# Optimization experiments

Hardware: AMD Instinct MI355X
Metric: run time of the kernel (lower is better)

Reference implementation:

```python
import jax, jax.numpy as jnp
import numpy as np

DIM = 16
HID = 256
BATCH = 8192
N_STEPS = 10      # fixed-step RK4 replaces adaptive dopri5 for a deterministic reference
T0, T1 = 0.0, 1.0
LOG_2PI = float(np.log(2.0 * np.pi))


def setup_inputs() -> dict:
    key = jax.random.key(0)
    ks = jax.random.split(key, 7)

    def lin_w(k, fan_in, fan_out):
        lim = 1.0 / np.sqrt(fan_in)
        return jax.random.uniform(k, (fan_in, fan_out), minval=-lim, maxval=lim, dtype=jnp.float32)

    def lin_b(k, fan_in, fan_out):
        lim = 1.0 / np.sqrt(fan_in)
        return jax.random.uniform(k, (fan_out,), minval=-lim, maxval=lim, dtype=jnp.float32)

    x = jax.random.normal(ks[0], (BATCH, DIM), dtype=jnp.float32)
    return {
        "x": x,
        "W1": lin_w(ks[1], DIM + 1, HID), "b1": lin_b(ks[2], DIM + 1, HID),
        "W2": lin_w(ks[3], HID, HID),     "b2": lin_b(ks[4], HID, HID),
        "W3": lin_w(ks[5], HID, DIM),     "b3": lin_b(ks[6], HID, DIM),
    }


def _mlp(W1, b1, W2, b2, W3, b3, h):
    h = jax.nn.silu(h @ W1 + b1)
    h = jax.nn.silu(h @ W2 + b2)
    return h @ W3 + b3


def reference(x, W1, b1, W2, b2, W3, b3):
    dtype = x.dtype

    def f(t, z):  # time-conditioned vector field f(z, t): [B, d] -> [B, d]
        t_col = jnp.full((z.shape[0], 1), t, dtype=dtype)
        return _mlp(W1, b1, W2, b2, W3, b3, jnp.concatenate([z, t_col], axis=1))

    eye = jnp.eye(DIM, dtype=dtype)

    def f_and_div(t, z):
        fz = f(t, z)
        # exact divergence = trace of Jacobian, via DIM forward-mode JVPs
        def jvp_dir(e):  # e: [d]
            _, jv = jax.jvp(lambda zz: f(t, zz), (z,), (jnp.broadcast_to(e, z.shape),))
            return jv  # [B, d]
        jvs = jax.vmap(jvp_dir)(eye)          # [d, B, d]
        div = jnp.einsum('ibi->b', jvs)       # sum_i dF_i/dz_i
        return fz, div

    dt = jnp.asarray((T1 - T0) / N_STEPS, dtype=dtype)

    def rhs(t, z):
        fz, div = f_and_div(t, z)
        return fz, -div   # dz/dt, dlogp/dt

    def step(state, i):
        z, logp = state
        t = T0 + i * dt
        k1z, k1l = rhs(t, z)
        k2z, k2l = rhs(t + 0.5 * dt, z + 0.5 * dt * k1z)
        k3z, k3l = rhs(t + 0.5 * dt, z + 0.5 * dt * k2z)
        k4z, k4l = rhs(t + dt, z + dt * k3z)
        z = z + (dt / 6.0) * (k1z + 2.0 * k2z + 2.0 * k3z + k4z)
        logp = logp + (dt / 6.0) * (k1l + 2.0 * k2l + 2.0 * k3l + k4l)
        return (z, logp), None

    logp0 = jnp.zeros(x.shape[0], dtype=dtype)
    (z1, logp1), _ = jax.lax.scan(step, (x, logp0), jnp.arange(N_STEPS, dtype=dtype))

    logpz = -0.5 * (jnp.sum(z1 * z1, axis=1) + DIM * LOG_2PI)
    return logpz - logp1
```

## Files before the change

kernel.cpp:

```cpp
#include <hip/hip_runtime.h>

#define DIM 16
#define HID 256
#define NSTEPS 10
#define TILE_B 32
#define NTHR 1024
#define LSH 264

typedef __attribute__((ext_vector_type(8))) short bf16x8;
typedef __attribute__((ext_vector_type(4))) float f32x4;

__device__ __forceinline__ unsigned short f2bf(float f) {
    unsigned u = __float_as_uint(f);
    u += 0x7fff + ((u >> 16) & 1);
    return (unsigned short)(u >> 16);
}
__device__ __forceinline__ unsigned short f2bf_trunc(float f) {
    return (unsigned short)(__float_as_uint(f) >> 16);
}
__device__ __forceinline__ float bf2f(unsigned short u) {
    return __uint_as_float((unsigned)u << 16);
}
__device__ __forceinline__ void silu_both(float x, float& h, float& d) {
    float s = __builtin_amdgcn_rcpf(1.0f + __expf(-x));
    h = x * s;
    d = fmaf(h, 1.0f - s, s);
}

__global__ void cnf_setup(const float* __restrict__ W1, const float* __restrict__ W2,
                          const float* __restrict__ W3,
                          unsigned short* __restrict__ w2t, unsigned short* __restrict__ mt) {
    const int j = blockIdx.x;
    const int n = threadIdx.x;
    float g = 0.0f;
#pragma unroll
    for (int i = 0; i < DIM; ++i) g = fmaf(W1[i * HID + j], W3[n * DIM + i], g);
    const float w2 = W2[j * HID + n];
    w2t[n * HID + j] = f2bf(w2);
    mt [n * HID + j] = f2bf(w2 * g);
}

__global__ __launch_bounds__(NTHR, 4) void cnf_main(
    const float* __restrict__ x,
    const float* __restrict__ W1, const float* __restrict__ b1,
    const float* __restrict__ b2, const float* __restrict__ b3,
    const unsigned short* __restrict__ w2t, const unsigned short* __restrict__ mt,
    const float* __restrict__ W3, float* __restrict__ out)
{
    __shared__ unsigned short zb[TILE_B][24];
    __shared__ unsigned short w1t[HID][24];
    __shared__ unsigned short w3t[DIM][LSH];
    __shared__ unsigned short h1s[TILE_B][LSH];
    __shared__ unsigned short d1s[TILE_B][LSH];
    __shared__ unsigned short h2s[TILE_B][LSH];
    __shared__ unsigned short d2s[TILE_B][LSH];
    __shared__ float divp[8][TILE_B];

    const int tid  = (int)threadIdx.x;
    const int lane = tid & 63;
    const int wv   = tid >> 6;
    const int g    = lane >> 4;
    const int r    = lane & 15;
    const int b0   = (int)blockIdx.x * TILE_B;
    const int wx   = (g >> 1) << 4;
    const int goff = (g * 8) ^ (((r >> 3) & 1) << 4);

    bf16x8 breg[8][2];
    const int n0w = (wv & 7) * 32;
    {
        const unsigned short* Bg = (wv < 8) ? w2t : mt;
#pragma unroll
        for (int k = 0; k < 8; ++k)
#pragma unroll
            for (int ct = 0; ct < 2; ++ct)
                breg[k][ct] = *(const bf16x8*)(Bg + (n0w + ct * 16 + r) * HID + k * 32 + g * 8);
    }

    const int n_p1 = wv * 16 + r;
    const int nw_p1 = n_p1 ^ wx;
    const float b1n = b1[n_p1];
    const float w1n = W1[DIM * HID + n_p1];
    const float b2r0 = b2[n0w + r], b2r1 = b2[n0w + 16 + r];
    float b3r = 0.0f;
    if (wv < 2) b3r = b3[r];

    if (tid < 512) {
        const int n = tid >> 1, kh = (tid & 1) * 8;
#pragma unroll
        for (int k = 0; k < 8; ++k) w1t[n][kh + k] = f2bf(W1[(kh + k) * HID + n]);
    }
    if (tid < 512) {
        const int n = tid >> 5, k0 = (tid & 31) * 8;
#pragma unroll
        for (int j = 0; j < 8; ++j) w3t[n][k0 + j] = f2bf(W3[(k0 + j) * DIM + n]);
    }
    float zb4[4] = {0.f, 0.f, 0.f, 0.f};
    float za4[4] = {0.f, 0.f, 0.f, 0.f};
    if (wv < 2) {
#pragma unroll
        for (int q = 0; q < 4; ++q) {
            const int row = wv * 16 + g * 4 + q;
            zb4[q] = x[(b0 + row) * DIM + r];
            zb[row][r] = f2bf(zb4[q]);
        }
    }
    float lacc = 0.0f, logp = 0.0f;

    const float dt = 0.1f, dt6 = dt / 6.0f;

    for (int it = 0; it < NSTEPS * 4; ++it) {
        const int s = it & 3;
        const int step = it >> 2;
        const float t0 = dt * (float)step;
        const float tcur = t0 + ((s == 0) ? 0.0f : (s == 3) ? dt : 0.5f * dt);
        const float wst = (s == 1 || s == 2) ? 2.0f : 1.0f;
        __syncthreads();

        if (wv == 8 && lane < 32 && it) {
            const int ps = (it + 3) & 3;
            const float pw = (ps == 1 || ps == 2) ? 2.0f : 1.0f;
            float dv = 0.0f;
#pragma unroll
            for (int w = 0; w < 8; ++w) dv += divp[w][lane];
            lacc = fmaf(-pw, dv, lacc);
            if (ps == 3) { logp = fmaf(dt6, lacc, logp); lacc = 0.0f; }
        }

        {
            const bf16x8 zf = {0, 0, 0, 0, 0, 0, 0, 0};
            bf16x8 az[2], bw;
#pragma unroll
            for (int rt = 0; rt < 2; ++rt)
                az[rt] = (g < 2) ? *(const bf16x8*)&zb[rt * 16 + r][g * 8] : zf;
            bw = (g < 2) ? *(const bf16x8*)&w1t[n_p1][g * 8] : zf;
            const float bb = fmaf(tcur, w1n, b1n);
#pragma unroll
            for (int rt = 0; rt < 2; ++rt) {
                f32x4 c = {0.f, 0.f, 0.f, 0.f};
                c = __builtin_amdgcn_mfma_f32_16x16x32_bf16(az[rt], bw, c, 0, 0, 0);
#pragma unroll
                for (int q = 0; q < 4; ++q) {
                    float h, d;
                    silu_both(c[q] + bb, h, d);
                    h1s[rt * 16 + g * 4 + q][nw_p1] = f2bf_trunc(h);
                    d1s[rt * 16 + g * 4 + q][nw_p1] = f2bf_trunc(d);
                }
            }
        }
        __syncthreads();

        f32x4 cc[2][2];
        {
            const unsigned short (*aT)[LSH] = (wv < 8) ? h1s : d1s;
#pragma unroll
            for (int a = 0; a < 2; ++a)
#pragma unroll
                for (int b = 0; b < 2; ++b) cc[a][b] = (f32x4){0.f, 0.f, 0.f, 0.f};
#pragma unroll
            for (int k = 0; k < 8; ++k) {
                bf16x8 af[2];
#pragma unroll
                for (int rt = 0; rt < 2; ++rt)
                    af[rt] = *(const bf16x8*)&aT[rt * 16 + r][k * 32 + goff];
#pragma unroll
                for (int rt = 0; rt < 2; ++rt)
#pragma unroll
                    for (int ct = 0; ct < 2; ++ct)
                        cc[rt][ct] = __builtin_amdgcn_mfma_f32_16x16x32_bf16(af[rt], breg[k][ct], cc[rt][ct], 0, 0, 0);
            }
        }
        if (wv < 8) {
#pragma unroll
            for (int ct = 0; ct < 2; ++ct) {
                const int nw = (n0w + ct * 16 + r) ^ wx;
                const float bb = (ct == 0) ? b2r0 : b2r1;
#pragma unroll
                for (int rt = 0; rt < 2; ++rt)
#pragma unroll
                    for (int q = 0; q < 4; ++q) {
                        float h, d;
                        silu_both(cc[rt][ct][q] + bb, h, d);
                        h2s[rt * 16 + g * 4 + q][nw] = f2bf_trunc(h);
                        d2s[rt * 16 + g * 4 + q][nw] = f2bf_trunc(d);
                    }
            }
        }
        __syncthreads();

        if (wv < 2) {
            f32x4 c3 = {0.f, 0.f, 0.f, 0.f};
#pragma unroll
            for (int ks = 0; ks < 8; ++ks) {
                bf16x8 a = *(const bf16x8*)&h2s[wv * 16 + r][ks * 32 + goff];
                bf16x8 b = *(const bf16x8*)&w3t[r][ks * 32 + g * 8];
                c3 = __builtin_amdgcn_mfma_f32_16x16x32_bf16(a, b, c3, 0, 0, 0);
            }
            const float coef = (s == 2) ? dt : 0.5f * dt;
#pragma unroll
            for (int q = 0; q < 4; ++q) {
                const float fz = c3[q] + b3r;
                za4[q] = fmaf(wst, fz, za4[q]);
                float znext;
                if (s < 3) {
                    znext = fmaf(coef, fz, zb4[q]);
                } else {
                    zb4[q] = fmaf(dt6, za4[q], zb4[q]);
                    znext = zb4[q];
                    za4[q] = 0.0f;
                }
                zb[wv * 16 + g * 4 + q][r] = f2bf(znext);
            }
        } else if (wv >= 8) {
            float p[2][4];
#pragma unroll
            for (int rt = 0; rt < 2; ++rt)
#pragma unroll
                for (int q = 0; q < 4; ++q) p[rt][q] = 0.0f;
#pragma unroll
            for (int ct = 0; ct < 2; ++ct) {
                const int nr = (n0w + ct * 16 + r) ^ wx;
#pragma unroll
                for (int rt = 0; rt < 2; ++rt)
#pragma unroll
                    for (int q = 0; q < 4; ++q) {
                        const float d2v = bf2f(d2s[rt * 16 + g * 4 + q][nr]);
                        p[rt][q] = fmaf(d2v, cc[rt][ct][q], p[rt][q]);
                    }
            }
#pragma unroll
            for (int m = 1; m < 16; m <<= 1)
#pragma unroll
                for (int rt = 0; rt < 2; ++rt)
#pragma unroll
                    for (int q = 0; q < 4; ++q) p[rt][q] += __shfl_xor(p[rt][q], m, 64);
            if (r == 0)
#pragma unroll
                for (int rt = 0; rt < 2; ++rt)
#pragma unroll
                    for (int q = 0; q < 4; ++q) divp[wv - 8][rt * 16 + g * 4 + q] = p[rt][q];
        }
    }

    __syncthreads();
    if (wv == 8 && lane < 32) {
        float dv = 0.0f;
#pragma unroll
        for (int w = 0; w < 8; ++w) dv += divp[w][lane];
        lacc -= dv;
        logp = fmaf(dt6, lacc, logp);
        divp[0][lane] = logp;
    }
    __syncthreads();
    if (wv < 2) {
        float ss[4];
#pragma unroll
        for (int q = 0; q < 4; ++q) ss[q] = zb4[q] * zb4[q];
#pragma unroll
        for (int m = 1; m < 16; m <<= 1)
#pragma unroll
            for (int q = 0; q < 4; ++q) ss[q] += __shfl_xor(ss[q], m, 64);
        if (r == 0) {
#pragma unroll
            for (int q = 0; q < 4; ++q) {
                const int row = wv * 16 + g * 4 + q;
                out[b0 + row] = -0.5f * (ss[q] + (float)DIM * 1.8378770664093453f) - divp[0][row];
            }
        }
    }
}

extern "C" void kernel_launch(void* const* d_in, const int* in_sizes, int n_in,
                              void* d_out, int out_size, void* d_ws, size_t ws_size,
                              hipStream_t stream) {
    (void)in_sizes; (void)n_in; (void)out_size; (void)ws_size;
    const float* x  = (const float*)d_in[0];
    const float* W1 = (const float*)d_in[1];
    const float* b1 = (const float*)d_in[2];
    const float* W2 = (const float*)d_in[3];
    const float* b2 = (const float*)d_in[4];
    const float* W3 = (const float*)d_in[5];
    const float* b3 = (const float*)d_in[6];
    unsigned short* w2t = (unsigned short*)d_ws;
    unsigned short* mt  = w2t + HID * HID;

    cnf_setup<<<HID, HID, 0, stream>>>(W1, W2, W3, w2t, mt);
    cnf_main<<<8192 / TILE_B, NTHR, 0, stream>>>(x, W1, b1, b2, b3, w2t, mt, W3, (float*)d_out);
}
```

Before: 218.4 us.

## Switch layer-2 to 32x32x16 MFMA with transposed operands and folded bias/time

Layer 2 now keeps the W2 and M weights as the A operand in registers and runs 32x32x16 MFMAs, giving one 16-float accumulator per wave in place of four 16x16 tiles. The divergence reduction then needs only a single cross-half shuffle instead of a 4-step butterfly. Layer 1 moves to the upper 8 waves, with time and b1 folded into the MFMA through an augmented z column, and its outputs are written as packed 4-element stores. The intent is fewer MFMA issues, fewer shuffles and fewer scalar LDS stores, at the cost of new swizzle patterns that could bring back bank conflicts.

```diff
diff --git a/kernel.cpp b/kernel.cpp
--- a/kernel.cpp
+++ b/kernel.cpp
@@ -9,17 +9,18 @@
 
 typedef __attribute__((ext_vector_type(8))) short bf16x8;
 typedef __attribute__((ext_vector_type(4))) float f32x4;
+typedef __attribute__((ext_vector_type(16))) float f32x16;
+typedef __attribute__((ext_vector_type(2))) unsigned int u32x2;
 
 __device__ __forceinline__ unsigned short f2bf(float f) {
     unsigned u = __float_as_uint(f);
     u += 0x7fff + ((u >> 16) & 1);
     return (unsigned short)(u >> 16);
 }
-__device__ __forceinline__ unsigned short f2bf_trunc(float f) {
-    return (unsigned short)(__float_as_uint(f) >> 16);
-}
-__device__ __forceinline__ float bf2f(unsigned short u) {
-    return __uint_as_float((unsigned)u << 16);
+__device__ __forceinline__ float bfw_lo(unsigned u) { return __uint_as_float(u << 16); }
+__device__ __forceinline__ float bfw_hi(unsigned u) { return __uint_as_float(u & 0xffff0000u); }
+__device__ __forceinline__ unsigned packtr(float a, float b) {
+    return __builtin_amdgcn_perm(__float_as_uint(b), __float_as_uint(a), 0x07060302u);
 }
 __device__ __forceinline__ void silu_both(float x, float& h, float& d) {
     float s = __builtin_amdgcn_rcpf(1.0f + __expf(-x));
@@ -47,76 +48,78 @@
     const unsigned short* __restrict__ w2t, const unsigned short* __restrict__ mt,
     const float* __restrict__ W3, float* __restrict__ out)
 {
-    __shared__ unsigned short zb[TILE_B][24];
-    __shared__ unsigned short w1t[HID][24];
+    __shared__ unsigned short zb[TILE_B][40];
     __shared__ unsigned short w3t[DIM][LSH];
     __shared__ unsigned short h1s[TILE_B][LSH];
     __shared__ unsigned short d1s[TILE_B][LSH];
     __shared__ unsigned short h2s[TILE_B][LSH];
     __shared__ unsigned short d2s[TILE_B][LSH];
     __shared__ float divp[8][TILE_B];
+    __shared__ float b2l[HID];
 
     const int tid  = (int)threadIdx.x;
     const int lane = tid & 63;
     const int wv   = tid >> 6;
-    const int g    = lane >> 4;
-    const int r    = lane & 15;
+    const int l5   = lane & 31, hi = lane >> 5, hi8 = hi * 8;
+    const int r    = lane & 15, g  = lane >> 4, g8  = g * 8;
     const int b0   = (int)blockIdx.x * TILE_B;
-    const int wx   = (g >> 1) << 4;
-    const int goff = (g * 8) ^ (((r >> 3) & 1) << 4);
-
-    bf16x8 breg[8][2];
-    const int n0w = (wv & 7) * 32;
+    const int swb  = ((l5 >> 3) & 1) << 4;
+    const int swr  = ((r  >> 3) & 1) << 4;
+    const int nblk = (wv & 7) * 32;
+
+    bf16x8 areg[16];
     {
-        const unsigned short* Bg = (wv < 8) ? w2t : mt;
-#pragma unroll
-        for (int k = 0; k < 8; ++k)
-#pragma unroll
-            for (int ct = 0; ct < 2; ++ct)
-                breg[k][ct] = *(const bf16x8*)(Bg + (n0w + ct * 16 + r) * HID + k * 32 + g * 8);
-    }
-
-    const int n_p1 = wv * 16 + r;
-    const int nw_p1 = n_p1 ^ wx;
-    const float b1n = b1[n_p1];
-    const float w1n = W1[DIM * HID + n_p1];
-    const float b2r0 = b2[n0w + r], b2r1 = b2[n0w + 16 + r];
-    float b3r = 0.0f;
-    if (wv < 2) b3r = b3[r];
-
-    if (tid < 512) {
-        const int n = tid >> 1, kh = (tid & 1) * 8;
-#pragma unroll
-        for (int k = 0; k < 8; ++k) w1t[n][kh + k] = f2bf(W1[(kh + k) * HID + n]);
+        const unsigned short* Arow = ((wv < 8) ? w2t : mt) + (nblk + l5) * HID + hi8;
+#pragma unroll
+        for (int kt = 0; kt < 16; ++kt) areg[kt] = *(const bf16x8*)(Arow + kt * 16);
+    }
+
+    bf16x8 w1f0 = {0,0,0,0,0,0,0,0}, w1f1 = {0,0,0,0,0,0,0,0};
+    if (wv >= 8) {
+        const int nb1 = (wv - 8) * 32;
+#pragma unroll
+        for (int e = 0; e < 8; ++e) {
+            const int k = g8 + e;
+            float v0 = 0.0f, v1 = 0.0f;
+            if (k < 17)       { v0 = W1[k * HID + nb1 + r]; v1 = W1[k * HID + nb1 + 16 + r]; }
+            else if (k == 17) { v0 = b1[nb1 + r];           v1 = b1[nb1 + 16 + r]; }
+            w1f0[e] = (short)f2bf(v0);
+            w1f1[e] = (short)f2bf(v1);
+        }
+    }
+
+    float zb4[4] = {0,0,0,0}, za4[4] = {0,0,0,0}, b3q[4] = {0,0,0,0};
+    if (wv < 2) {
+#pragma unroll
+        for (int q = 0; q < 4; ++q) b3q[q] = b3[4 * g + q];
+        const f32x4 xv = *(const f32x4*)&x[(b0 + wv * 16 + r) * DIM + 4 * g];
+#pragma unroll
+        for (int q = 0; q < 4; ++q) zb4[q] = xv[q];
+        u32x2 pz = { (unsigned)f2bf(zb4[0]) | ((unsigned)f2bf(zb4[1]) << 16),
+                     (unsigned)f2bf(zb4[2]) | ((unsigned)f2bf(zb4[3]) << 16) };
+        *(u32x2*)&zb[wv * 16 + r][4 * g] = pz;
+    }
+    if (tid < TILE_B) {
+#pragma unroll
+        for (int c = 16; c < 32; ++c)
+            zb[tid][c] = (c == 17) ? (unsigned short)0x3F80 : (unsigned short)0;
     }
     if (tid < 512) {
         const int n = tid >> 5, k0 = (tid & 31) * 8;
 #pragma unroll
         for (int j = 0; j < 8; ++j) w3t[n][k0 + j] = f2bf(W3[(k0 + j) * DIM + n]);
     }
-    float zb4[4] = {0.f, 0.f, 0.f, 0.f};
-    float za4[4] = {0.f, 0.f, 0.f, 0.f};
-    if (wv < 2) {
-#pragma unroll
-        for (int q = 0; q < 4; ++q) {
-            const int row = wv * 16 + g * 4 + q;
-            zb4[q] = x[(b0 + row) * DIM + r];
-            zb[row][r] = f2bf(zb4[q]);
-        }
-    }
+    if (tid < HID) b2l[tid] = b2[tid];
+
     float lacc = 0.0f, logp = 0.0f;
-
     const float dt = 0.1f, dt6 = dt / 6.0f;
 
     for (int it = 0; it < NSTEPS * 4; ++it) {
         const int s = it & 3;
-        const int step = it >> 2;
-        const float t0 = dt * (float)step;
-        const float tcur = t0 + ((s == 0) ? 0.0f : (s == 3) ? dt : 0.5f * dt);
         const float wst = (s == 1 || s == 2) ? 2.0f : 1.0f;
         __syncthreads();
 
-        if (wv == 8 && lane < 32 && it) {
+        if (wv == 8 && lane < TILE_B && it) {
             const int ps = (it + 3) & 3;
             const float pw = (ps == 1 || ps == 2) ? 2.0f : 1.0f;
             float dv = 0.0f;
@@ -126,123 +129,102 @@
             if (ps == 3) { logp = fmaf(dt6, lacc, logp); lacc = 0.0f; }
         }
 
+        if (wv >= 8) {
+            const int nb1 = (wv - 8) * 32;
+#pragma unroll
+            for (int bt = 0; bt < 2; ++bt) {
+                const bf16x8 bz = *(const bf16x8*)&zb[bt * 16 + r][g8];
+#pragma unroll
+                for (int nt = 0; nt < 2; ++nt) {
+                    f32x4 c = {0.f, 0.f, 0.f, 0.f};
+                    c = __builtin_amdgcn_mfma_f32_16x16x32_bf16(nt ? w1f1 : w1f0, bz, c, 0, 0, 0);
+                    float h[4], d[4];
+#pragma unroll
+                    for (int q = 0; q < 4; ++q) silu_both(c[q], h[q], d[q]);
+                    const int col = (nb1 + nt * 16 + 4 * g) ^ swr;
+                    const int row = bt * 16 + r;
+                    u32x2 hv = { packtr(h[0], h[1]), packtr(h[2], h[3]) };
+                    u32x2 dv2 = { packtr(d[0], d[1]), packtr(d[2], d[3]) };
+                    *(u32x2*)&h1s[row][col] = hv;
+                    *(u32x2*)&d1s[row][col] = dv2;
+                }
+            }
+        }
+        __syncthreads();
+
+        f32x16 cc;
+#pragma unroll
+        for (int p = 0; p < 16; ++p) cc[p] = 0.0f;
         {
-            const bf16x8 zf = {0, 0, 0, 0, 0, 0, 0, 0};
-            bf16x8 az[2], bw;
-#pragma unroll
-            for (int rt = 0; rt < 2; ++rt)
-                az[rt] = (g < 2) ? *(const bf16x8*)&zb[rt * 16 + r][g * 8] : zf;
-            bw = (g < 2) ? *(const bf16x8*)&w1t[n_p1][g * 8] : zf;
-            const float bb = fmaf(tcur, w1n, b1n);
-#pragma unroll
-            for (int rt = 0; rt < 2; ++rt) {
-                f32x4 c = {0.f, 0.f, 0.f, 0.f};
-                c = __builtin_amdgcn_mfma_f32_16x16x32_bf16(az[rt], bw, c, 0, 0, 0);
-#pragma unroll
-                for (int q = 0; q < 4; ++q) {
-                    float h, d;
-                    silu_both(c[q] + bb, h, d);
-                    h1s[rt * 16 + g * 4 + q][nw_p1] = f2bf_trunc(h);
-                    d1s[rt * 16 + g * 4 + q][nw_p1] = f2bf_trunc(d);
-                }
-            }
-        }
-        __syncthreads();
-
-        f32x4 cc[2][2];
-        {
-            const unsigned short (*aT)[LSH] = (wv < 8) ? h1s : d1s;
-#pragma unroll
-            for (int a = 0; a < 2; ++a)
-#pragma unroll
-                for (int b = 0; b < 2; ++b) cc[a][b] = (f32x4){0.f, 0.f, 0.f, 0.f};
-#pragma unroll
-            for (int k = 0; k < 8; ++k) {
-                bf16x8 af[2];
-#pragma unroll
-                for (int rt = 0; rt < 2; ++rt)
-                    af[rt] = *(const bf16x8*)&aT[rt * 16 + r][k * 32 + goff];
-#pragma unroll
-                for (int rt = 0; rt < 2; ++rt)
-#pragma unroll
-                    for (int ct = 0; ct < 2; ++ct)
-                        cc[rt][ct] = __builtin_amdgcn_mfma_f32_16x16x32_bf16(af[rt], breg[k][ct], cc[rt][ct], 0, 0, 0);
+            const unsigned short* Brow = (wv < 8) ? &h1s[l5][0] : &d1s[l5][0];
+#pragma unroll
+            for (int kt = 0; kt < 16; ++kt) {
+                const bf16x8 bf = *(const bf16x8*)(Brow + ((kt * 16 + hi8) ^ swb));
+                cc = __builtin_amdgcn_mfma_f32_32x32x16_bf16(areg[kt], bf, cc, 0, 0, 0);
             }
         }
         if (wv < 8) {
 #pragma unroll
-            for (int ct = 0; ct < 2; ++ct) {
-                const int nw = (n0w + ct * 16 + r) ^ wx;
-                const float bb = (ct == 0) ? b2r0 : b2r1;
-#pragma unroll
-                for (int rt = 0; rt < 2; ++rt)
-#pragma unroll
-                    for (int q = 0; q < 4; ++q) {
-                        float h, d;
-                        silu_both(cc[rt][ct][q] + bb, h, d);
-                        h2s[rt * 16 + g * 4 + q][nw] = f2bf_trunc(h);
-                        d2s[rt * 16 + g * 4 + q][nw] = f2bf_trunc(d);
-                    }
+            for (int pg = 0; pg < 4; ++pg) {
+                const f32x4 bb = *(const f32x4*)&b2l[nblk + pg * 8 + 4 * hi];
+                float h[4], d[4];
+#pragma unroll
+                for (int q = 0; q < 4; ++q) silu_both(cc[pg * 4 + q] + bb[q], h[q], d[q]);
+                const int col = (nblk + pg * 8 + 4 * hi) ^ swb;
+                u32x2 hv = { packtr(h[0], h[1]), packtr(h[2], h[3]) };
+                u32x2 dv2 = { packtr(d[0], d[1]), packtr(d[2], d[3]) };
+                *(u32x2*)&h2s[l5][col] = hv;
+                *(u32x2*)&d2s[l5][col] = dv2;
             }
         }
         __syncthreads();
 
         if (wv < 2) {
             f32x4 c3 = {0.f, 0.f, 0.f, 0.f};
-#pragma unroll
-            for (int ks = 0; ks < 8; ++ks) {
-                bf16x8 a = *(const bf16x8*)&h2s[wv * 16 + r][ks * 32 + goff];
-                bf16x8 b = *(const bf16x8*)&w3t[r][ks * 32 + g * 8];
-                c3 = __builtin_amdgcn_mfma_f32_16x16x32_bf16(a, b, c3, 0, 0, 0);
+            const unsigned short* h2row = &h2s[wv * 16 + r][0];
+            const unsigned short* w3row = &w3t[r][0];
+#pragma unroll
+            for (int kt = 0; kt < 8; ++kt) {
+                const bf16x8 a3  = *(const bf16x8*)(w3row + kt * 32 + g8);
+                const bf16x8 bf3 = *(const bf16x8*)(h2row + ((kt * 32 + g8) ^ swr));
+                c3 = __builtin_amdgcn_mfma_f32_16x16x32_bf16(a3, bf3, c3, 0, 0, 0);
             }
             const float coef = (s == 2) ? dt : 0.5f * dt;
+            float zn[4];
 #pragma unroll
             for (int q = 0; q < 4; ++q) {
-                const float fz = c3[q] + b3r;
+                const float fz = c3[q] + b3q[q];
                 za4[q] = fmaf(wst, fz, za4[q]);
-                float znext;
-                if (s < 3) {
-                    znext = fmaf(coef, fz, zb4[q]);
-                } else {
-                    zb4[q] = fmaf(dt6, za4[q], zb4[q]);
-                    znext = zb4[q];
-                    za4[q] = 0.0f;
-                }
-                zb[wv * 16 + g * 4 + q][r] = f2bf(znext);
+                if (s < 3) zn[q] = fmaf(coef, fz, zb4[q]);
+                else { zb4[q] = fmaf(dt6, za4[q], zb4[q]); zn[q] = zb4[q]; za4[q] = 0.0f; }
+            }
+            u32x2 pz = { (unsigned)f2bf(zn[0]) | ((unsigned)f2bf(zn[1]) << 16),
+                         (unsigned)f2bf(zn[2]) | ((unsigned)f2bf(zn[3]) << 16) };
+            *(u32x2*)&zb[wv * 16 + r][4 * g] = pz;
+            if (wv == 0 && lane < TILE_B) {
+                const int it1 = it + 1;
+                const int s1 = it1 & 3;
+                const float t1 = dt * (float)(it1 >> 2) + ((s1 == 0) ? 0.0f : (s1 == 3) ? dt : 0.5f * dt);
+                zb[lane][16] = f2bf(t1);
             }
         } else if (wv >= 8) {
-            float p[2][4];
-#pragma unroll
-            for (int rt = 0; rt < 2; ++rt)
-#pragma unroll
-                for (int q = 0; q < 4; ++q) p[rt][q] = 0.0f;
-#pragma unroll
-            for (int ct = 0; ct < 2; ++ct) {
-                const int nr = (n0w + ct * 16 + r) ^ wx;
-#pragma unroll
-                for (int rt = 0; rt < 2; ++rt)
-#pragma unroll
-                    for (int q = 0; q < 4; ++q) {
-                        const float d2v = bf2f(d2s[rt * 16 + g * 4 + q][nr]);
-                        p[rt][q] = fmaf(d2v, cc[rt][ct][q], p[rt][q]);
-                    }
-            }
-#pragma unroll
-            for (int m = 1; m < 16; m <<= 1)
-#pragma unroll
-                for (int rt = 0; rt < 2; ++rt)
-#pragma unroll
-                    for (int q = 0; q < 4; ++q) p[rt][q] += __shfl_xor(p[rt][q], m, 64);
-            if (r == 0)
-#pragma unroll
-                for (int rt = 0; rt < 2; ++rt)
-#pragma unroll
-                    for (int q = 0; q < 4; ++q) divp[wv - 8][rt * 16 + g * 4 + q] = p[rt][q];
+            float pd = 0.0f;
+#pragma unroll
+            for (int pg = 0; pg < 4; ++pg) {
+                const int col = (nblk + pg * 8 + 4 * hi) ^ swb;
+                const u32x2 du = *(const u32x2*)&d2s[l5][col];
+                pd = fmaf(bfw_lo(du[0]), cc[pg * 4 + 0], pd);
+                pd = fmaf(bfw_hi(du[0]), cc[pg * 4 + 1], pd);
+                pd = fmaf(bfw_lo(du[1]), cc[pg * 4 + 2], pd);
+                pd = fmaf(bfw_hi(du[1]), cc[pg * 4 + 3], pd);
+            }
+            pd += __shfl_xor(pd, 32, 64);
+            if (lane < TILE_B) divp[wv - 8][lane] = pd;
         }
     }
 
     __syncthreads();
-    if (wv == 8 && lane < 32) {
+    if (wv == 8 && lane < TILE_B) {
         float dv = 0.0f;
 #pragma unroll
         for (int w = 0; w < 8; ++w) dv += divp[w][lane];
@@ -252,19 +234,12 @@
     }
     __syncthreads();
     if (wv < 2) {
-        float ss[4];
-#pragma unroll
-        for (int q = 0; q < 4; ++q) ss[q] = zb4[q] * zb4[q];
-#pragma unroll
-        for (int m = 1; m < 16; m <<= 1)
-#pragma unroll
-            for (int q = 0; q < 4; ++q) ss[q] += __shfl_xor(ss[q], m, 64);
-        if (r == 0) {
-#pragma unroll
-            for (int q = 0; q < 4; ++q) {
-                const int row = wv * 16 + g * 4 + q;
-                out[b0 + row] = -0.5f * (ss[q] + (float)DIM * 1.8378770664093453f) - divp[0][row];
-            }
+        float ss = zb4[0]*zb4[0] + zb4[1]*zb4[1] + zb4[2]*zb4[2] + zb4[3]*zb4[3];
+        ss += __shfl_xor(ss, 16, 64);
+        ss += __shfl_xor(ss, 32, 64);
+        if (g == 0) {
+            const int row = wv * 16 + r;
+            out[b0 + row] = -0.5f * (ss + (float)DIM * 1.8378770664093453f) - divp[0][row];
         }
     }
 }
```

Result: slower. 307.4 us (+40.8%).

## Transpose MFMA operands and fold time and bias into layer-1 GEMM

Applied to the files above, without the earlier changes.

Layer 1 now swaps the MFMA operands so each lane holds four consecutive hidden columns. This allows packed 64-bit stores of h1/d1 via byte-permute truncation. The time input and the b1 bias are folded into the K dimension as extra columns (t and a constant 1) held in zb, with W1 kept in registers instead of shared memory. Layer 3 is likewise transposed so z is written as packed vectors, and it uses two accumulators to break the MFMA dependency chain. The final reduction needs fewer shuffles. The risk is that t and b1 are now rounded to bf16, which slightly changes accuracy.

```diff
diff --git a/kernel.cpp b/kernel.cpp
--- a/kernel.cpp
+++ b/kernel.cpp
@@ -9,6 +9,7 @@
 
 typedef __attribute__((ext_vector_type(8))) short bf16x8;
 typedef __attribute__((ext_vector_type(4))) float f32x4;
+typedef __attribute__((ext_vector_type(2))) unsigned int u32x2;
 
 __device__ __forceinline__ unsigned short f2bf(float f) {
     unsigned u = __float_as_uint(f);
@@ -20,6 +21,9 @@
 }
 __device__ __forceinline__ float bf2f(unsigned short u) {
     return __uint_as_float((unsigned)u << 16);
+}
+__device__ __forceinline__ unsigned packtr(float a, float b) {
+    return __builtin_amdgcn_perm(__float_as_uint(b), __float_as_uint(a), 0x07060302u);
 }
 __device__ __forceinline__ void silu_both(float x, float& h, float& d) {
     float s = __builtin_amdgcn_rcpf(1.0f + __expf(-x));
@@ -47,8 +51,7 @@
     const unsigned short* __restrict__ w2t, const unsigned short* __restrict__ mt,
     const float* __restrict__ W3, float* __restrict__ out)
 {
-    __shared__ unsigned short zb[TILE_B][24];
-    __shared__ unsigned short w1t[HID][24];
+    __shared__ unsigned short zb[TILE_B][40];
     __shared__ unsigned short w3t[DIM][LSH];
     __shared__ unsigned short h1s[TILE_B][LSH];
     __shared__ unsigned short d1s[TILE_B][LSH];
@@ -61,62 +64,71 @@
     const int wv   = tid >> 6;
     const int g    = lane >> 4;
     const int r    = lane & 15;
+    const int g8   = g * 8;
     const int b0   = (int)blockIdx.x * TILE_B;
     const int wx   = (g >> 1) << 4;
-    const int goff = (g * 8) ^ (((r >> 3) & 1) << 4);
+    const int swr  = ((r >> 3) & 1) << 4;
+    const int goff = g8 ^ swr;
+    const int n0w  = (wv & 7) * 32;
 
     bf16x8 breg[8][2];
-    const int n0w = (wv & 7) * 32;
     {
         const unsigned short* Bg = (wv < 8) ? w2t : mt;
 #pragma unroll
         for (int k = 0; k < 8; ++k)
 #pragma unroll
             for (int ct = 0; ct < 2; ++ct)
-                breg[k][ct] = *(const bf16x8*)(Bg + (n0w + ct * 16 + r) * HID + k * 32 + g * 8);
-    }
-
-    const int n_p1 = wv * 16 + r;
-    const int nw_p1 = n_p1 ^ wx;
-    const float b1n = b1[n_p1];
-    const float w1n = W1[DIM * HID + n_p1];
+                breg[k][ct] = *(const bf16x8*)(Bg + (n0w + ct * 16 + r) * HID + k * 32 + g8);
+    }
+
+    bf16x8 w1f;
+    {
+        const int n = wv * 16 + r;
+#pragma unroll
+        for (int e = 0; e < 8; ++e) {
+            const int k = g8 + e;
+            float v = 0.0f;
+            if (k < 17)       v = W1[k * HID + n];
+            else if (k == 17) v = b1[n];
+            w1f[e] = (short)f2bf(v);
+        }
+    }
+
     const float b2r0 = b2[n0w + r], b2r1 = b2[n0w + 16 + r];
-    float b3r = 0.0f;
-    if (wv < 2) b3r = b3[r];
-
-    if (tid < 512) {
-        const int n = tid >> 1, kh = (tid & 1) * 8;
-#pragma unroll
-        for (int k = 0; k < 8; ++k) w1t[n][kh + k] = f2bf(W1[(kh + k) * HID + n]);
+    float b3q[4] = {0, 0, 0, 0};
+    if (wv < 2)
+#pragma unroll
+        for (int q = 0; q < 4; ++q) b3q[q] = b3[4 * g + q];
+
+    float zb4[4] = {0, 0, 0, 0}, za4[4] = {0, 0, 0, 0};
+    if (wv < 2) {
+        const f32x4 xv = *(const f32x4*)&x[(b0 + wv * 16 + r) * DIM + 4 * g];
+#pragma unroll
+        for (int q = 0; q < 4; ++q) zb4[q] = xv[q];
+        u32x2 pz = { (unsigned)f2bf(zb4[0]) | ((unsigned)f2bf(zb4[1]) << 16),
+                     (unsigned)f2bf(zb4[2]) | ((unsigned)f2bf(zb4[3]) << 16) };
+        *(u32x2*)&zb[wv * 16 + r][4 * g] = pz;
+    }
+    if (tid < TILE_B) {
+#pragma unroll
+        for (int c = 16; c < 32; ++c)
+            zb[tid][c] = (c == 17) ? (unsigned short)0x3F80 : (unsigned short)0;
     }
     if (tid < 512) {
         const int n = tid >> 5, k0 = (tid & 31) * 8;
 #pragma unroll
         for (int j = 0; j < 8; ++j) w3t[n][k0 + j] = f2bf(W3[(k0 + j) * DIM + n]);
     }
-    float zb4[4] = {0.f, 0.f, 0.f, 0.f};
-    float za4[4] = {0.f, 0.f, 0.f, 0.f};
-    if (wv < 2) {
-#pragma unroll
-        for (int q = 0; q < 4; ++q) {
-            const int row = wv * 16 + g * 4 + q;
-            zb4[q] = x[(b0 + row) * DIM + r];
-            zb[row][r] = f2bf(zb4[q]);
-        }
-    }
+
     float lacc = 0.0f, logp = 0.0f;
-
     const float dt = 0.1f, dt6 = dt / 6.0f;
 
     for (int it = 0; it < NSTEPS * 4; ++it) {
         const int s = it & 3;
-        const int step = it >> 2;
-        const float t0 = dt * (float)step;
-        const float tcur = t0 + ((s == 0) ? 0.0f : (s == 3) ? dt : 0.5f * dt);
         const float wst = (s == 1 || s == 2) ? 2.0f : 1.0f;
         __syncthreads();
 
-        if (wv == 8 && lane < 32 && it) {
+        if (wv == 8 && lane < TILE_B && it) {
             const int ps = (it + 3) & 3;
             const float pw = (ps == 1 || ps == 2) ? 2.0f : 1.0f;
             float dv = 0.0f;
@@ -127,24 +139,20 @@
         }
 
         {
-            const bf16x8 zf = {0, 0, 0, 0, 0, 0, 0, 0};
-            bf16x8 az[2], bw;
-#pragma unroll
-            for (int rt = 0; rt < 2; ++rt)
-                az[rt] = (g < 2) ? *(const bf16x8*)&zb[rt * 16 + r][g * 8] : zf;
-            bw = (g < 2) ? *(const bf16x8*)&w1t[n_p1][g * 8] : zf;
-            const float bb = fmaf(tcur, w1n, b1n);
-#pragma unroll
-            for (int rt = 0; rt < 2; ++rt) {
+#pragma unroll
+            for (int bt = 0; bt < 2; ++bt) {
+                const bf16x8 bz = *(const bf16x8*)&zb[bt * 16 + r][g8];
                 f32x4 c = {0.f, 0.f, 0.f, 0.f};
-                c = __builtin_amdgcn_mfma_f32_16x16x32_bf16(az[rt], bw, c, 0, 0, 0);
-#pragma unroll
-                for (int q = 0; q < 4; ++q) {
-                    float h, d;
-                    silu_both(c[q] + bb, h, d);
-                    h1s[rt * 16 + g * 4 + q][nw_p1] = f2bf_trunc(h);
-                    d1s[rt * 16 + g * 4 + q][nw_p1] = f2bf_trunc(d);
-                }
+                c = __builtin_amdgcn_mfma_f32_16x16x32_bf16(w1f, bz, c, 0, 0, 0);
+                float h[4], d[4];
+#pragma unroll
+                for (int q = 0; q < 4; ++q) silu_both(c[q], h[q], d[q]);
+                const int row = bt * 16 + r;
+                const int col = (wv * 16 + 4 * g) ^ swr;
+                u32x2 hv  = { packtr(h[0], h[1]), packtr(h[2], h[3]) };
+                u32x2 dv2 = { packtr(d[0], d[1]), packtr(d[2], d[3]) };
+                *(u32x2*)&h1s[row][col] = hv;
+                *(u32x2*)&d1s[row][col] = dv2;
             }
         }
         __syncthreads();
@@ -188,27 +196,33 @@
         __syncthreads();
 
         if (wv < 2) {
-            f32x4 c3 = {0.f, 0.f, 0.f, 0.f};
-#pragma unroll
-            for (int ks = 0; ks < 8; ++ks) {
-                bf16x8 a = *(const bf16x8*)&h2s[wv * 16 + r][ks * 32 + goff];
-                bf16x8 b = *(const bf16x8*)&w3t[r][ks * 32 + g * 8];
-                c3 = __builtin_amdgcn_mfma_f32_16x16x32_bf16(a, b, c3, 0, 0, 0);
+            const unsigned short* h2row = &h2s[wv * 16 + r][0];
+            const unsigned short* w3row = &w3t[r][0];
+            f32x4 c3a = {0.f, 0.f, 0.f, 0.f}, c3b = {0.f, 0.f, 0.f, 0.f};
+#pragma unroll
+            for (int kt = 0; kt < 8; ++kt) {
+                const bf16x8 a3  = *(const bf16x8*)(w3row + kt * 32 + g8);
+                const bf16x8 bf3 = *(const bf16x8*)(h2row + kt * 32 + goff);
+                if (kt & 1) c3b = __builtin_amdgcn_mfma_f32_16x16x32_bf16(a3, bf3, c3b, 0, 0, 0);
+                else        c3a = __builtin_amdgcn_mfma_f32_16x16x32_bf16(a3, bf3, c3a, 0, 0, 0);
             }
             const float coef = (s == 2) ? dt : 0.5f * dt;
+            float zn[4];
 #pragma unroll
             for (int q = 0; q < 4; ++q) {
-                const float fz = c3[q] + b3r;
+                const float fz = c3a[q] + c3b[q] + b3q[q];
                 za4[q] = fmaf(wst, fz, za4[q]);
-                float znext;
-                if (s < 3) {
-                    znext = fmaf(coef, fz, zb4[q]);
-                } else {
-                    zb4[q] = fmaf(dt6, za4[q], zb4[q]);
-                    znext = zb4[q];
-                    za4[q] = 0.0f;
-                }
-                zb[wv * 16 + g * 4 + q][r] = f2bf(znext);
+                if (s < 3) zn[q] = fmaf(coef, fz, zb4[q]);
+                else { zb4[q] = fmaf(dt6, za4[q], zb4[q]); zn[q] = zb4[q]; za4[q] = 0.0f; }
+            }
+            u32x2 pz = { (unsigned)f2bf(zn[0]) | ((unsigned)f2bf(zn[1]) << 16),
+                         (unsigned)f2bf(zn[2]) | ((unsigned)f2bf(zn[3]) << 16) };
+            *(u32x2*)&zb[wv * 16 + r][4 * g] = pz;
+            if (wv == 0 && lane < TILE_B) {
+                const int it1 = it + 1;
+                const int s1 = it1 & 3;
+                const float t1 = dt * (float)(it1 >> 2) + ((s1 == 0) ? 0.0f : (s1 == 3) ? dt : 0.5f * dt);
+                zb[lane][16] = f2bf(t1);
             }
         } else if (wv >= 8) {
             float p[2][4];
@@ -242,7 +256,7 @@
     }
 
     __syncthreads();
-    if (wv == 8 && lane < 32) {
+    if (wv == 8 && lane < TILE_B) {
         float dv = 0.0f;
 #pragma unroll
         for (int w = 0; w < 8; ++w) dv += divp[w][lane];
@@ -252,19 +266,12 @@
     }
     __syncthreads();
     if (wv < 2) {
-        float ss[4];
-#pragma unroll
-        for (int q = 0; q < 4; ++q) ss[q] = zb4[q] * zb4[q];
-#pragma unroll
-        for (int m = 1; m < 16; m <<= 1)
-#pragma unroll
-            for (int q = 0; q < 4; ++q) ss[q] += __shfl_xor(ss[q], m, 64);
-        if (r == 0) {
-#pragma unroll
-            for (int q = 0; q < 4; ++q) {
-                const int row = wv * 16 + g * 4 + q;
-                out[b0 + row] = -0.5f * (ss[q] + (float)DIM * 1.8378770664093453f) - divp[0][row];
-            }
+        float ss = zb4[0] * zb4[0] + zb4[1] * zb4[1] + zb4[2] * zb4[2] + zb4[3] * zb4[3];
+        ss += __shfl_xor(ss, 16, 64);
+        ss += __shfl_xor(ss, 32, 64);
+        if (g == 0) {
+            const int row = wv * 16 + r;
+            out[b0 + row] = -0.5f * (ss + (float)DIM * 1.8378770664093453f) - divp[0][row];
         }
     }
 }
```

New measurement: 218.2 us. Within noise of the previous version (-0.1%).
